# Optimization experiments

Measured on AMD Instinct MI355X. Metric: run time of the kernel, lower is better.

Reference implementation:

```python
import jax, jax.numpy as jnp
import numpy as np

A_CONST = 0.4
C_CONST = 500.0
N_BINS = 10


def entropy(w):
    # Faithful to the torch helper: n=10 half-open bins [min+i*s, min+(i+1)*s);
    # the maximum element falls outside the last bin, as in the original.
    x = w.reshape(-1)
    lo = x.min()
    hi = x.max()
    scale = (hi - lo) / N_BINS
    i = jnp.arange(N_BINS, dtype=x.dtype)
    lower = lo + i * scale            # [n]
    upper = lo + (i + 1.0) * scale    # [n]
    in_bin = (x[None, :] >= lower[:, None]) & (x[None, :] < upper[:, None])  # [n, len]
    p = jnp.sum(in_bin, axis=1).astype(jnp.float32) / x.shape[0]
    return jnp.sum(jnp.where(p > 0, -p * jnp.log(p), 0.0))


def blend_weight(base_w, graft_w, pnet_w):
    # param_direction = |base - graft| passed through bias-free Linear(in, in)
    d = jnp.abs(base_w - graft_w) @ pnet_w.T          # [out, in]
    w_local = jax.nn.sigmoid(d)
    w_global = A_CONST / jnp.pi * jnp.arctan(C_CONST * (entropy(base_w) - entropy(graft_w))) + 0.5
    w_base = w_global * (1.0 - jnp.exp(-w_global * w_local))
    w_graft = (1.0 - w_global) * (1.0 - jnp.exp(-(1.0 - w_global) * (1.0 - w_local)))
    ws = jax.nn.softmax(jnp.stack([w_base, w_graft], axis=-1), axis=-1)  # [out, in, 2]
    return base_w * ws[..., 0] + graft_w * ws[..., 1]


def setup_inputs() -> dict:
    key = jax.random.key(0)
    ks = jax.random.split(key, 9)
    B, D_IN, D_H, D_OUT = 65536, 1024, 512, 1
    return {
        "x": jax.random.normal(ks[0], (B, D_IN), dtype=jnp.float32),
        "w0": jax.random.normal(ks[1], (D_H, D_IN), dtype=jnp.float32) * 0.05,
        "b0": jax.random.normal(ks[2], (D_H,), dtype=jnp.float32) * 0.05,
        "w1": jax.random.normal(ks[3], (D_OUT, D_H), dtype=jnp.float32) * 0.05,
        "b1": jax.random.normal(ks[4], (D_OUT,), dtype=jnp.float32) * 0.05,
        "p0": jax.random.normal(ks[5], (D_IN, D_IN), dtype=jnp.float32) * 0.05,
        "p1": jax.random.normal(ks[6], (D_H, D_H), dtype=jnp.float32) * 0.05,
        "g0": jax.random.normal(ks[7], (D_H, D_IN), dtype=jnp.float32) * 0.05,
        "g1": jax.random.normal(ks[8], (D_OUT, D_H), dtype=jnp.float32) * 0.05,
    }


def reference(x, w0, b0, w1, b1, p0, p1, g0, g1):
    W0 = blend_weight(w0, g0, p0)
    x = jax.nn.relu(x @ W0.T + b0)   # layer 0 + ReLU
    W1 = blend_weight(w1, g1, p1)
    x = x @ W1.T + b1                # layer 1, no activation
    return x
```

## Files before the change

### kernel.cpp

```cpp
#include <hip/hip_runtime.h>
#include <hip/hip_bf16.h>
#include <math.h>


typedef __attribute__((ext_vector_type(8))) short short8;
typedef __attribute__((ext_vector_type(4))) float floatx4;
typedef unsigned short ushort_t;

#define WS_ENT 0
#define WS_MM 4
#define WS_CNT 16
#define WS_W0B_WORD 64
#define WS_W1B_WORD (64 + 262144)

__device__ __forceinline__ unsigned f2ord(float f) {
    unsigned u = __float_as_uint(f);
    return (u & 0x80000000u) ? ~u : (u | 0x80000000u);
}
__device__ __forceinline__ float ord2f(unsigned k) {
    unsigned u = (k & 0x80000000u) ? (k ^ 0x80000000u) : ~k;
    return __uint_as_float(u);
}
__device__ __forceinline__ short f2bf(float f) {
    union { __hip_bfloat16 h; short s; } u;
    u.h = __float2bfloat16(f);
    return u.s;
}
__device__ __forceinline__ float blend_factor(float d, float wg) {
    float wl = 1.0f / (1.0f + expf(-d));
    float wb = wg * (1.0f - expf(-wg * wl));
    float wgr = (1.0f - wg) * (1.0f - expf(-(1.0f - wg) * (1.0f - wl)));
    return 1.0f / (1.0f + expf(-(wb - wgr)));
}
__device__ __forceinline__ float wglobal_from_ent(float eb, float eg) {
    return 0.12732395447351627f * atanf(500.0f * (eb - eg)) + 0.5f;
}
__device__ __forceinline__ void async16(const void* g, void* s) {
    __builtin_amdgcn_global_load_lds(
        (const __attribute__((address_space(1))) unsigned int*)g,
        (__attribute__((address_space(3))) unsigned int*)s, 16, 0, 0);
}

__global__ void init_kernel(unsigned* ws_u, float* out, const float* __restrict__ b1) {
    int gid = blockIdx.x * 256 + threadIdx.x;
    out[gid] = b1[0];
    if (blockIdx.x == 0) {
        int t = threadIdx.x;
        if (t < 4) {
            ws_u[WS_MM + 2 * t] = 0xFFFFFFFFu;
            ws_u[WS_MM + 2 * t + 1] = 0u;
        }
        if (t >= WS_CNT && t < WS_CNT + 40) ws_u[t] = 0u;
    }
}

__device__ __forceinline__ void array_map(int bx, const float* w0, const float* g0,
                                          const float* w1, const float* g1,
                                          int& a, const float*& arr, int& per, int& start) {
    if (bx < 64) { a = 0; arr = w0; per = 524288 / 64; start = bx * per; }
    else if (bx < 128) { a = 1; arr = g0; per = 524288 / 64; start = (bx - 64) * per; }
    else if (bx == 128) { a = 2; arr = w1; per = 512; start = 0; }
    else { a = 3; arr = g1; per = 512; start = 0; }
}

__global__ __launch_bounds__(256) void minmax_kernel(const float* __restrict__ w0,
                                                     const float* __restrict__ g0,
                                                     const float* __restrict__ w1,
                                                     const float* __restrict__ g1,
                                                     unsigned* ws_u) {
    int a, per, start;
    const float* arr;
    array_map(blockIdx.x, w0, g0, w1, g1, a, arr, per, start);
    float mn = INFINITY, mx = -INFINITY;
    for (int i = threadIdx.x; i < per; i += 256) {
        float v = arr[start + i];
        mn = fminf(mn, v);
        mx = fmaxf(mx, v);
    }
#pragma unroll
    for (int off = 32; off > 0; off >>= 1) {
        mn = fminf(mn, __shfl_xor(mn, off));
        mx = fmaxf(mx, __shfl_xor(mx, off));
    }
    __shared__ float smn[4], smx[4];
    int wave = threadIdx.x >> 6, lane = threadIdx.x & 63;
    if (lane == 0) { smn[wave] = mn; smx[wave] = mx; }
    __syncthreads();
    if (threadIdx.x == 0) {
        mn = fminf(fminf(smn[0], smn[1]), fminf(smn[2], smn[3]));
        mx = fmaxf(fmaxf(smx[0], smx[1]), fmaxf(smx[2], smx[3]));
        atomicMin(&ws_u[WS_MM + 2 * a], f2ord(mn));
        atomicMax(&ws_u[WS_MM + 2 * a + 1], f2ord(mx));
    }
}

__global__ __launch_bounds__(256) void hist_kernel(const float* __restrict__ w0,
                                                   const float* __restrict__ g0,
                                                   const float* __restrict__ w1,
                                                   const float* __restrict__ g1,
                                                   unsigned* ws_u) {
    int a, per, start;
    const float* arr;
    array_map(blockIdx.x, w0, g0, w1, g1, a, arr, per, start);
    float lo = ord2f(ws_u[WS_MM + 2 * a]);
    float hi = ord2f(ws_u[WS_MM + 2 * a + 1]);
    float scale = __fdiv_rn(__fsub_rn(hi, lo), 10.0f);
    __shared__ float lower[11];
    __shared__ unsigned cnt[10];
    if (threadIdx.x < 11)
        lower[threadIdx.x] = __fadd_rn(lo, __fmul_rn((float)threadIdx.x, scale));
    if (threadIdx.x < 10) cnt[threadIdx.x] = 0u;
    __syncthreads();
    float inv_scale = 1.0f / scale;
    for (int i = threadIdx.x; i < per; i += 256) {
        float v = arr[start + i];
        int g = (int)floorf((v - lo) * inv_scale);
#pragma unroll
        for (int db = -1; db <= 1; db++) {
            int b = g + db;
            if (b >= 0 && b <= 9 && v >= lower[b] && v < lower[b + 1])
                atomicAdd(&cnt[b], 1u);
        }
    }
    __syncthreads();
    if (threadIdx.x < 10 && cnt[threadIdx.x] > 0)
        atomicAdd(&ws_u[WS_CNT + a * 10 + threadIdx.x], cnt[threadIdx.x]);
}

__global__ void finalize_ent_kernel(unsigned* ws_u) {
    int a = threadIdx.x;
    if (a < 4) {
        float n = (a < 2) ? 524288.0f : 512.0f;
        float ent = 0.0f;
        for (int i = 0; i < 10; i++) {
            float p = __fdiv_rn((float)ws_u[WS_CNT + a * 10 + i], n);
            if (p > 0.0f) ent = __fsub_rn(ent, __fmul_rn(p, logf(p)));
        }
        ((float*)ws_u)[WS_ENT + a] = ent;
    }
}

__global__ __launch_bounds__(256) void blend0_kernel(const float* __restrict__ w0,
                                                     const float* __restrict__ g0,
                                                     const float* __restrict__ p0,
                                                     const float* __restrict__ ws_f,
                                                     ushort_t* __restrict__ W0bb) {
    __shared__ float As[64][17];
    __shared__ float Bs[64][17];
    int tid = threadIdx.x;
    int bo = blockIdx.y * 64;
    int bi = blockIdx.x * 64;
    int tx = tid & 15, ty = tid >> 4;
    int lr = tid >> 2, lc = (tid & 3) * 4;
    float acc[4][4] = {};
    for (int k0 = 0; k0 < 1024; k0 += 16) {
        float4 vw = *(const float4*)&w0[(bo + lr) * 1024 + k0 + lc];
        float4 vg = *(const float4*)&g0[(bo + lr) * 1024 + k0 + lc];
        float4 vp = *(const float4*)&p0[(bi + lr) * 1024 + k0 + lc];
        As[lr][lc + 0] = fabsf(vw.x - vg.x);
        As[lr][lc + 1] = fabsf(vw.y - vg.y);
        As[lr][lc + 2] = fabsf(vw.z - vg.z);
        As[lr][lc + 3] = fabsf(vw.w - vg.w);
        Bs[lr][lc + 0] = vp.x;
        Bs[lr][lc + 1] = vp.y;
        Bs[lr][lc + 2] = vp.z;
        Bs[lr][lc + 3] = vp.w;
        __syncthreads();
#pragma unroll
        for (int k = 0; k < 16; k++) {
            float av[4], bv[4];
#pragma unroll
            for (int r = 0; r < 4; r++) av[r] = As[ty * 4 + r][k];
#pragma unroll
            for (int c = 0; c < 4; c++) bv[c] = Bs[tx * 4 + c][k];
#pragma unroll
            for (int r = 0; r < 4; r++)
#pragma unroll
                for (int c = 0; c < 4; c++) acc[r][c] += av[r] * bv[c];
        }
        __syncthreads();
    }
    float wg = wglobal_from_ent(ws_f[WS_ENT + 0], ws_f[WS_ENT + 1]);
#pragma unroll
    for (int r = 0; r < 4; r++) {
#pragma unroll
        for (int c = 0; c < 4; c++) {
            int o = bo + ty * 4 + r, i = bi + tx * 4 + c;
            float s0 = blend_factor(acc[r][c], wg);
            float v = w0[o * 1024 + i] * s0 + g0[o * 1024 + i] * (1.0f - s0);
            W0bb[o * 1024 + i] = (ushort_t)f2bf(v);
        }
    }
}

__global__ __launch_bounds__(256) void blend1_kernel(const float* __restrict__ w1,
                                                     const float* __restrict__ g1,
                                                     const float* __restrict__ p1,
                                                     const float* __restrict__ ws_f,
                                                     float* __restrict__ W1b) {
    __shared__ float diff[512];
    int tid = threadIdx.x;
    for (int i = tid; i < 512; i += 256) diff[i] = fabsf(w1[i] - g1[i]);
    __syncthreads();
    int wave = tid >> 6, lane = tid & 63;
    int i = blockIdx.x * 4 + wave;
    float acc = 0.0f;
#pragma unroll
    for (int j = 0; j < 8; j++) {
        int k = lane + 64 * j;
        acc += diff[k] * p1[i * 512 + k];
    }
#pragma unroll
    for (int off = 32; off > 0; off >>= 1) acc += __shfl_xor(acc, off);
    if (lane == 0) {
        float wg = wglobal_from_ent(ws_f[WS_ENT + 2], ws_f[WS_ENT + 3]);
        float s0 = blend_factor(acc, wg);
        W1b[i] = w1[i] * s0 + g1[i] * (1.0f - s0);
    }
}

__global__ __launch_bounds__(256) void main_mfma(const float* __restrict__ x,
                                                 const float* __restrict__ b0,
                                                 const ushort_t* __restrict__ W0bb,
                                                 const float* __restrict__ W1b,
                                                 float* __restrict__ out) {
    __shared__ ushort_t As[128 * 40];
    __shared__ ushort_t Bs[128 * 32];
    int tid = threadIdx.x;
    int w = tid >> 6, l = tid & 63;
    int row0 = blockIdx.x * 128, col0 = blockIdx.y * 128;
    int wm = w & 1, wn = w >> 1;
    int m_in = l & 15, kq = l >> 4;

    floatx4 acc[4][4];
    const floatx4 zero = {0.0f, 0.0f, 0.0f, 0.0f};
#pragma unroll
    for (int tm = 0; tm < 4; tm++)
#pragma unroll
        for (int tn = 0; tn < 4; tn++) acc[tm][tn] = zero;

    int arow = tid >> 1;
    int acol = (tid & 1) * 16;
    const float* xbase = x + (size_t)(row0 + arow) * 1024 + acol;
    ushort_t* awr = &As[arow * 40 + acol];
    const ushort_t* bsrc0 = W0bb + (size_t)(col0 + w * 16 + (l >> 2)) * 1024 + (l & 3) * 8;
    const ushort_t* bsrc1 = bsrc0 + (size_t)64 * 1024;
    ushort_t* bdst0 = &Bs[w * 512];
    ushort_t* bdst1 = &Bs[2048 + w * 512];

#pragma unroll 1
    for (int k0 = 0; k0 < 1024; k0 += 32) {
        async16(bsrc0 + k0, bdst0);
        async16(bsrc1 + k0, bdst1);
        float4 v0 = *(const float4*)(xbase + k0);
        float4 v1 = *(const float4*)(xbase + k0 + 4);
        float4 v2 = *(const float4*)(xbase + k0 + 8);
        float4 v3 = *(const float4*)(xbase + k0 + 12);
        short8 s0, s1;
        s0[0] = f2bf(v0.x); s0[1] = f2bf(v0.y); s0[2] = f2bf(v0.z); s0[3] = f2bf(v0.w);
        s0[4] = f2bf(v1.x); s0[5] = f2bf(v1.y); s0[6] = f2bf(v1.z); s0[7] = f2bf(v1.w);
        s1[0] = f2bf(v2.x); s1[1] = f2bf(v2.y); s1[2] = f2bf(v2.z); s1[3] = f2bf(v2.w);
        s1[4] = f2bf(v3.x); s1[5] = f2bf(v3.y); s1[6] = f2bf(v3.z); s1[7] = f2bf(v3.w);
        *(short8*)(awr) = s0;
        *(short8*)(awr + 8) = s1;
        __syncthreads();
        short8 af[4], bfr[4];
#pragma unroll
        for (int tm = 0; tm < 4; tm++)
            af[tm] = *(const short8*)&As[(wm * 64 + tm * 16 + m_in) * 40 + kq * 8];
#pragma unroll
        for (int tn = 0; tn < 4; tn++)
            bfr[tn] = *(const short8*)&Bs[(wn * 64 + tn * 16 + m_in) * 32 + kq * 8];
#pragma unroll
        for (int tm = 0; tm < 4; tm++)
#pragma unroll
            for (int tn = 0; tn < 4; tn++)
                acc[tm][tn] = __builtin_amdgcn_mfma_f32_16x16x32_bf16(
                    af[tm], bfr[tn], acc[tm][tn], 0, 0, 0);
        __syncthreads();
    }

    float b0v[4], w1v[4];
#pragma unroll
    for (int tn = 0; tn < 4; tn++) {
        int h = col0 + wn * 64 + tn * 16 + m_in;
        b0v[tn] = b0[h];
        w1v[tn] = W1b[h];
    }
#pragma unroll
    for (int tm = 0; tm < 4; tm++) {
#pragma unroll
        for (int reg = 0; reg < 4; reg++) {
            float s = 0.0f;
#pragma unroll
            for (int tn = 0; tn < 4; tn++) {
                float y = acc[tm][tn][reg] + b0v[tn];
                y = fmaxf(y, 0.0f);
                s += y * w1v[tn];
            }
            s += __shfl_xor(s, 1);
            s += __shfl_xor(s, 2);
            s += __shfl_xor(s, 4);
            s += __shfl_xor(s, 8);
            if (m_in == 0)
                atomicAdd(&out[row0 + wm * 64 + tm * 16 + kq * 4 + reg], s);
        }
    }
}

extern "C" void kernel_launch(void* const* d_in, const int* in_sizes, int n_in,
                              void* d_out, int out_size, void* d_ws, size_t ws_size,
                              hipStream_t stream) {
    const float* x = (const float*)d_in[0];
    const float* w0 = (const float*)d_in[1];
    const float* b0 = (const float*)d_in[2];
    const float* w1 = (const float*)d_in[3];
    const float* b1 = (const float*)d_in[4];
    const float* p0 = (const float*)d_in[5];
    const float* p1 = (const float*)d_in[6];
    const float* g0 = (const float*)d_in[7];
    const float* g1 = (const float*)d_in[8];
    float* out = (float*)d_out;
    unsigned* ws_u = (unsigned*)d_ws;
    float* ws_f = (float*)d_ws;
    ushort_t* W0bb = (ushort_t*)(ws_u + WS_W0B_WORD);
    float* W1b = ws_f + WS_W1B_WORD;

    init_kernel<<<256, 256, 0, stream>>>(ws_u, out, b1);
    minmax_kernel<<<130, 256, 0, stream>>>(w0, g0, w1, g1, ws_u);
    hist_kernel<<<130, 256, 0, stream>>>(w0, g0, w1, g1, ws_u);
    finalize_ent_kernel<<<1, 64, 0, stream>>>(ws_u);
    blend0_kernel<<<dim3(16, 8), 256, 0, stream>>>(w0, g0, p0, ws_f, W0bb);
    blend1_kernel<<<128, 256, 0, stream>>>(w1, g1, p1, ws_f, W1b);
    main_mfma<<<dim3(512, 4), 256, 0, stream>>>(x, b0, W0bb, W1b, out);
}
```

Before: 627.4 us.

## Fuse prep stages into cooperative kernel and widen main GEMM tile to full hidden dim

Merges the init, min/max, histogram, entropy and both blend kernels into one cooperative kernel separated by grid-wide syncs, cutting five launches. The main MFMA kernel now gives each block 64 rows across all 512 hidden units, with a swizzled LDS layout for W0 and register prefetch of x. The layer-1 dot product is reduced in shared memory and written directly, replacing global atomics and the output init pass. In exchange it adds grid-sync overhead, raises LDS and register use per block (fewer resident blocks), and each block now streams the whole W0 matrix.

```diff
diff --git a/kernel.cpp b/kernel.cpp
--- a/kernel.cpp
+++ b/kernel.cpp
@@ -1,6 +1,9 @@
 #include <hip/hip_runtime.h>
 #include <hip/hip_bf16.h>
+#include <hip/hip_cooperative_groups.h>
 #include <math.h>
+
+namespace cg = cooperative_groups;
 
 
 typedef __attribute__((ext_vector_type(8))) short short8;
@@ -39,19 +42,6 @@
     __builtin_amdgcn_global_load_lds(
         (const __attribute__((address_space(1))) unsigned int*)g,
         (__attribute__((address_space(3))) unsigned int*)s, 16, 0, 0);
-}
-
-__global__ void init_kernel(unsigned* ws_u, float* out, const float* __restrict__ b1) {
-    int gid = blockIdx.x * 256 + threadIdx.x;
-    out[gid] = b1[0];
-    if (blockIdx.x == 0) {
-        int t = threadIdx.x;
-        if (t < 4) {
-            ws_u[WS_MM + 2 * t] = 0xFFFFFFFFu;
-            ws_u[WS_MM + 2 * t + 1] = 0u;
-        }
-        if (t >= WS_CNT && t < WS_CNT + 40) ws_u[t] = 0u;
-    }
 }
 
 __device__ __forceinline__ void array_map(int bx, const float* w0, const float* g0,
@@ -63,227 +53,232 @@
     else { a = 3; arr = g1; per = 512; start = 0; }
 }
 
-__global__ __launch_bounds__(256) void minmax_kernel(const float* __restrict__ w0,
-                                                     const float* __restrict__ g0,
-                                                     const float* __restrict__ w1,
-                                                     const float* __restrict__ g1,
-                                                     unsigned* ws_u) {
-    int a, per, start;
-    const float* arr;
-    array_map(blockIdx.x, w0, g0, w1, g1, a, arr, per, start);
-    float mn = INFINITY, mx = -INFINITY;
-    for (int i = threadIdx.x; i < per; i += 256) {
-        float v = arr[start + i];
-        mn = fminf(mn, v);
-        mx = fmaxf(mx, v);
-    }
-#pragma unroll
-    for (int off = 32; off > 0; off >>= 1) {
-        mn = fminf(mn, __shfl_xor(mn, off));
-        mx = fmaxf(mx, __shfl_xor(mx, off));
-    }
+__global__ __launch_bounds__(256) void prep_kernel(
+    const float* __restrict__ w0, const float* __restrict__ g0,
+    const float* __restrict__ w1, const float* __restrict__ g1,
+    const float* __restrict__ p0, const float* __restrict__ p1,
+    unsigned* ws_u, ushort_t* __restrict__ W0bb, float* __restrict__ W1b) {
+    cg::grid_group grid = cg::this_grid();
+    float* ws_f = (float*)ws_u;
+    int bx = blockIdx.x, tid = threadIdx.x;
+    int wave = tid >> 6, lane = tid & 63;
+
     __shared__ float smn[4], smx[4];
-    int wave = threadIdx.x >> 6, lane = threadIdx.x & 63;
-    if (lane == 0) { smn[wave] = mn; smx[wave] = mx; }
-    __syncthreads();
-    if (threadIdx.x == 0) {
-        mn = fminf(fminf(smn[0], smn[1]), fminf(smn[2], smn[3]));
-        mx = fmaxf(fmaxf(smx[0], smx[1]), fmaxf(smx[2], smx[3]));
-        atomicMin(&ws_u[WS_MM + 2 * a], f2ord(mn));
-        atomicMax(&ws_u[WS_MM + 2 * a + 1], f2ord(mx));
-    }
-}
-
-__global__ __launch_bounds__(256) void hist_kernel(const float* __restrict__ w0,
-                                                   const float* __restrict__ g0,
-                                                   const float* __restrict__ w1,
-                                                   const float* __restrict__ g1,
-                                                   unsigned* ws_u) {
-    int a, per, start;
-    const float* arr;
-    array_map(blockIdx.x, w0, g0, w1, g1, a, arr, per, start);
-    float lo = ord2f(ws_u[WS_MM + 2 * a]);
-    float hi = ord2f(ws_u[WS_MM + 2 * a + 1]);
-    float scale = __fdiv_rn(__fsub_rn(hi, lo), 10.0f);
     __shared__ float lower[11];
     __shared__ unsigned cnt[10];
-    if (threadIdx.x < 11)
-        lower[threadIdx.x] = __fadd_rn(lo, __fmul_rn((float)threadIdx.x, scale));
-    if (threadIdx.x < 10) cnt[threadIdx.x] = 0u;
-    __syncthreads();
-    float inv_scale = 1.0f / scale;
-    for (int i = threadIdx.x; i < per; i += 256) {
-        float v = arr[start + i];
-        int g = (int)floorf((v - lo) * inv_scale);
-#pragma unroll
-        for (int db = -1; db <= 1; db++) {
-            int b = g + db;
-            if (b >= 0 && b <= 9 && v >= lower[b] && v < lower[b + 1])
-                atomicAdd(&cnt[b], 1u);
-        }
-    }
-    __syncthreads();
-    if (threadIdx.x < 10 && cnt[threadIdx.x] > 0)
-        atomicAdd(&ws_u[WS_CNT + a * 10 + threadIdx.x], cnt[threadIdx.x]);
-}
-
-__global__ void finalize_ent_kernel(unsigned* ws_u) {
-    int a = threadIdx.x;
-    if (a < 4) {
+    __shared__ float diff[512];
+    __shared__ float As[64][17];
+    __shared__ float Bs[64][17];
+
+    if (bx == 0) {
+        if (tid < 4) {
+            ws_u[WS_MM + 2 * tid] = 0xFFFFFFFFu;
+            ws_u[WS_MM + 2 * tid + 1] = 0u;
+        }
+        if (tid >= WS_CNT && tid < WS_CNT + 40) ws_u[tid] = 0u;
+    }
+    grid.sync();
+
+    {
+        int a, per, start;
+        const float* arr;
+        array_map(bx, w0, g0, w1, g1, a, arr, per, start);
+        float mn = INFINITY, mx = -INFINITY;
+        for (int i = tid; i < per; i += 256) {
+            float v = arr[start + i];
+            mn = fminf(mn, v);
+            mx = fmaxf(mx, v);
+        }
+#pragma unroll
+        for (int off = 32; off > 0; off >>= 1) {
+            mn = fminf(mn, __shfl_xor(mn, off));
+            mx = fmaxf(mx, __shfl_xor(mx, off));
+        }
+        if (lane == 0) { smn[wave] = mn; smx[wave] = mx; }
+        __syncthreads();
+        if (tid == 0) {
+            mn = fminf(fminf(smn[0], smn[1]), fminf(smn[2], smn[3]));
+            mx = fmaxf(fmaxf(smx[0], smx[1]), fmaxf(smx[2], smx[3]));
+            atomicMin(&ws_u[WS_MM + 2 * a], f2ord(mn));
+            atomicMax(&ws_u[WS_MM + 2 * a + 1], f2ord(mx));
+        }
+    }
+    grid.sync();
+
+    {
+        int a, per, start;
+        const float* arr;
+        array_map(bx, w0, g0, w1, g1, a, arr, per, start);
+        float lo = ord2f(ws_u[WS_MM + 2 * a]);
+        float hi = ord2f(ws_u[WS_MM + 2 * a + 1]);
+        float scale = __fdiv_rn(__fsub_rn(hi, lo), 10.0f);
+        if (tid < 11) lower[tid] = __fadd_rn(lo, __fmul_rn((float)tid, scale));
+        if (tid < 10) cnt[tid] = 0u;
+        __syncthreads();
+        float inv_scale = 1.0f / scale;
+        for (int i = tid; i < per; i += 256) {
+            float v = arr[start + i];
+            int g = (int)floorf((v - lo) * inv_scale);
+#pragma unroll
+            for (int db = -1; db <= 1; db++) {
+                int b = g + db;
+                if (b >= 0 && b <= 9 && v >= lower[b] && v < lower[b + 1])
+                    atomicAdd(&cnt[b], 1u);
+            }
+        }
+        __syncthreads();
+        if (tid < 10 && cnt[tid] > 0)
+            atomicAdd(&ws_u[WS_CNT + a * 10 + tid], cnt[tid]);
+    }
+    grid.sync();
+
+    if (bx == 0 && tid < 4) {
+        int a = tid;
         float n = (a < 2) ? 524288.0f : 512.0f;
         float ent = 0.0f;
         for (int i = 0; i < 10; i++) {
             float p = __fdiv_rn((float)ws_u[WS_CNT + a * 10 + i], n);
             if (p > 0.0f) ent = __fsub_rn(ent, __fmul_rn(p, logf(p)));
         }
-        ((float*)ws_u)[WS_ENT + a] = ent;
-    }
-}
-
-__global__ __launch_bounds__(256) void blend0_kernel(const float* __restrict__ w0,
-                                                     const float* __restrict__ g0,
-                                                     const float* __restrict__ p0,
-                                                     const float* __restrict__ ws_f,
-                                                     ushort_t* __restrict__ W0bb) {
-    __shared__ float As[64][17];
-    __shared__ float Bs[64][17];
-    int tid = threadIdx.x;
-    int bo = blockIdx.y * 64;
-    int bi = blockIdx.x * 64;
-    int tx = tid & 15, ty = tid >> 4;
-    int lr = tid >> 2, lc = (tid & 3) * 4;
-    float acc[4][4] = {};
-    for (int k0 = 0; k0 < 1024; k0 += 16) {
-        float4 vw = *(const float4*)&w0[(bo + lr) * 1024 + k0 + lc];
-        float4 vg = *(const float4*)&g0[(bo + lr) * 1024 + k0 + lc];
-        float4 vp = *(const float4*)&p0[(bi + lr) * 1024 + k0 + lc];
-        As[lr][lc + 0] = fabsf(vw.x - vg.x);
-        As[lr][lc + 1] = fabsf(vw.y - vg.y);
-        As[lr][lc + 2] = fabsf(vw.z - vg.z);
-        As[lr][lc + 3] = fabsf(vw.w - vg.w);
-        Bs[lr][lc + 0] = vp.x;
-        Bs[lr][lc + 1] = vp.y;
-        Bs[lr][lc + 2] = vp.z;
-        Bs[lr][lc + 3] = vp.w;
-        __syncthreads();
-#pragma unroll
-        for (int k = 0; k < 16; k++) {
-            float av[4], bv[4];
-#pragma unroll
-            for (int r = 0; r < 4; r++) av[r] = As[ty * 4 + r][k];
-#pragma unroll
-            for (int c = 0; c < 4; c++) bv[c] = Bs[tx * 4 + c][k];
-#pragma unroll
-            for (int r = 0; r < 4; r++)
-#pragma unroll
-                for (int c = 0; c < 4; c++) acc[r][c] += av[r] * bv[c];
-        }
-        __syncthreads();
-    }
-    float wg = wglobal_from_ent(ws_f[WS_ENT + 0], ws_f[WS_ENT + 1]);
-#pragma unroll
-    for (int r = 0; r < 4; r++) {
-#pragma unroll
-        for (int c = 0; c < 4; c++) {
-            int o = bo + ty * 4 + r, i = bi + tx * 4 + c;
-            float s0 = blend_factor(acc[r][c], wg);
-            float v = w0[o * 1024 + i] * s0 + g0[o * 1024 + i] * (1.0f - s0);
-            W0bb[o * 1024 + i] = (ushort_t)f2bf(v);
-        }
-    }
-}
-
-__global__ __launch_bounds__(256) void blend1_kernel(const float* __restrict__ w1,
-                                                     const float* __restrict__ g1,
-                                                     const float* __restrict__ p1,
-                                                     const float* __restrict__ ws_f,
-                                                     float* __restrict__ W1b) {
-    __shared__ float diff[512];
-    int tid = threadIdx.x;
-    for (int i = tid; i < 512; i += 256) diff[i] = fabsf(w1[i] - g1[i]);
-    __syncthreads();
-    int wave = tid >> 6, lane = tid & 63;
-    int i = blockIdx.x * 4 + wave;
-    float acc = 0.0f;
-#pragma unroll
-    for (int j = 0; j < 8; j++) {
-        int k = lane + 64 * j;
-        acc += diff[k] * p1[i * 512 + k];
-    }
-#pragma unroll
-    for (int off = 32; off > 0; off >>= 1) acc += __shfl_xor(acc, off);
-    if (lane == 0) {
-        float wg = wglobal_from_ent(ws_f[WS_ENT + 2], ws_f[WS_ENT + 3]);
-        float s0 = blend_factor(acc, wg);
-        W1b[i] = w1[i] * s0 + g1[i] * (1.0f - s0);
-    }
-}
-
-__global__ __launch_bounds__(256) void main_mfma(const float* __restrict__ x,
-                                                 const float* __restrict__ b0,
-                                                 const ushort_t* __restrict__ W0bb,
-                                                 const float* __restrict__ W1b,
-                                                 float* __restrict__ out) {
-    __shared__ ushort_t As[128 * 40];
-    __shared__ ushort_t Bs[128 * 32];
+        ws_f[WS_ENT + a] = ent;
+    }
+    grid.sync();
+
+    if (bx < 128) {
+        for (int i = tid; i < 512; i += 256) diff[i] = fabsf(w1[i] - g1[i]);
+        __syncthreads();
+        int i = bx * 4 + wave;
+        float acc = 0.0f;
+#pragma unroll
+        for (int j = 0; j < 8; j++) {
+            int k = lane + 64 * j;
+            acc += diff[k] * p1[i * 512 + k];
+        }
+#pragma unroll
+        for (int off = 32; off > 0; off >>= 1) acc += __shfl_xor(acc, off);
+        if (lane == 0) {
+            float wg = wglobal_from_ent(ws_f[WS_ENT + 2], ws_f[WS_ENT + 3]);
+            float s0 = blend_factor(acc, wg);
+            W1b[i] = w1[i] * s0 + g1[i] * (1.0f - s0);
+        }
+        __syncthreads();
+    }
+
+    if (bx < 128) {
+        int bo = (bx >> 4) * 64;
+        int bi = (bx & 15) * 64;
+        int tx = tid & 15, ty = tid >> 4;
+        int lr = tid >> 2, lc = (tid & 3) * 4;
+        float acc[4][4] = {};
+        for (int k0 = 0; k0 < 1024; k0 += 16) {
+            float4 vw = *(const float4*)&w0[(bo + lr) * 1024 + k0 + lc];
+            float4 vg = *(const float4*)&g0[(bo + lr) * 1024 + k0 + lc];
+            float4 vp = *(const float4*)&p0[(bi + lr) * 1024 + k0 + lc];
+            As[lr][lc + 0] = fabsf(vw.x - vg.x);
+            As[lr][lc + 1] = fabsf(vw.y - vg.y);
+            As[lr][lc + 2] = fabsf(vw.z - vg.z);
+            As[lr][lc + 3] = fabsf(vw.w - vg.w);
+            Bs[lr][lc + 0] = vp.x;
+            Bs[lr][lc + 1] = vp.y;
+            Bs[lr][lc + 2] = vp.z;
+            Bs[lr][lc + 3] = vp.w;
+            __syncthreads();
+#pragma unroll
+            for (int k = 0; k < 16; k++) {
+                float av[4], bv[4];
+#pragma unroll
+                for (int r = 0; r < 4; r++) av[r] = As[ty * 4 + r][k];
+#pragma unroll
+                for (int c = 0; c < 4; c++) bv[c] = Bs[tx * 4 + c][k];
+#pragma unroll
+                for (int r = 0; r < 4; r++)
+#pragma unroll
+                    for (int c = 0; c < 4; c++) acc[r][c] += av[r] * bv[c];
+            }
+            __syncthreads();
+        }
+        float wg = wglobal_from_ent(ws_f[WS_ENT + 0], ws_f[WS_ENT + 1]);
+#pragma unroll
+        for (int r = 0; r < 4; r++) {
+#pragma unroll
+            for (int c = 0; c < 4; c++) {
+                int o = bo + ty * 4 + r, i = bi + tx * 4 + c;
+                float s0 = blend_factor(acc[r][c], wg);
+                float v = w0[o * 1024 + i] * s0 + g0[o * 1024 + i] * (1.0f - s0);
+                W0bb[o * 1024 + i] = (ushort_t)f2bf(v);
+            }
+        }
+    }
+}
+
+__global__ __launch_bounds__(256) void main_mfma(
+    const float* __restrict__ x, const float* __restrict__ b0,
+    const float* __restrict__ b1, const ushort_t* __restrict__ W0bb,
+    const float* __restrict__ W1b, float* __restrict__ out) {
+    __shared__ ushort_t As[64 * 40];
+    __shared__ ushort_t Bs[512 * 32];
+    __shared__ float red[4 * 64];
+
     int tid = threadIdx.x;
     int w = tid >> 6, l = tid & 63;
-    int row0 = blockIdx.x * 128, col0 = blockIdx.y * 128;
-    int wm = w & 1, wn = w >> 1;
     int m_in = l & 15, kq = l >> 4;
-
-    floatx4 acc[4][4];
+    int row0 = blockIdx.x * 64;
+
+    floatx4 acc[4][8];
     const floatx4 zero = {0.0f, 0.0f, 0.0f, 0.0f};
 #pragma unroll
     for (int tm = 0; tm < 4; tm++)
 #pragma unroll
-        for (int tn = 0; tn < 4; tn++) acc[tm][tn] = zero;
-
-    int arow = tid >> 1;
-    int acol = (tid & 1) * 16;
-    const float* xbase = x + (size_t)(row0 + arow) * 1024 + acol;
-    ushort_t* awr = &As[arow * 40 + acol];
-    const ushort_t* bsrc0 = W0bb + (size_t)(col0 + w * 16 + (l >> 2)) * 1024 + (l & 3) * 8;
-    const ushort_t* bsrc1 = bsrc0 + (size_t)64 * 1024;
-    ushort_t* bdst0 = &Bs[w * 512];
-    ushort_t* bdst1 = &Bs[2048 + w * 512];
+        for (int tn = 0; tn < 8; tn++) acc[tm][tn] = zero;
+
+    int ar = tid >> 2, akc = (tid & 3) * 8;
+    const float* xptr = x + (size_t)(row0 + ar) * 1024 + akc;
+    ushort_t* awr = &As[ar * 40 + akc];
+
+    int c_src = ((l & 3) - (l >> 3)) & 3;
+    const ushort_t* bsrc = W0bb + (size_t)(w * 16 + (l >> 2)) * 1024 + c_src * 8;
+    ushort_t* bdst = &Bs[w * 512];
+
+    float4 xa = *(const float4*)(xptr);
+    float4 xb = *(const float4*)(xptr + 4);
 
 #pragma unroll 1
     for (int k0 = 0; k0 < 1024; k0 += 32) {
-        async16(bsrc0 + k0, bdst0);
-        async16(bsrc1 + k0, bdst1);
-        float4 v0 = *(const float4*)(xbase + k0);
-        float4 v1 = *(const float4*)(xbase + k0 + 4);
-        float4 v2 = *(const float4*)(xbase + k0 + 8);
-        float4 v3 = *(const float4*)(xbase + k0 + 12);
-        short8 s0, s1;
-        s0[0] = f2bf(v0.x); s0[1] = f2bf(v0.y); s0[2] = f2bf(v0.z); s0[3] = f2bf(v0.w);
-        s0[4] = f2bf(v1.x); s0[5] = f2bf(v1.y); s0[6] = f2bf(v1.z); s0[7] = f2bf(v1.w);
-        s1[0] = f2bf(v2.x); s1[1] = f2bf(v2.y); s1[2] = f2bf(v2.z); s1[3] = f2bf(v2.w);
-        s1[4] = f2bf(v3.x); s1[5] = f2bf(v3.y); s1[6] = f2bf(v3.z); s1[7] = f2bf(v3.w);
-        *(short8*)(awr) = s0;
-        *(short8*)(awr + 8) = s1;
-        __syncthreads();
-        short8 af[4], bfr[4];
+#pragma unroll
+        for (int i = 0; i < 8; i++)
+            async16(bsrc + i * 65536 + k0, bdst + i * 2048);
+        short8 s8;
+        s8[0] = f2bf(xa.x); s8[1] = f2bf(xa.y); s8[2] = f2bf(xa.z); s8[3] = f2bf(xa.w);
+        s8[4] = f2bf(xb.x); s8[5] = f2bf(xb.y); s8[6] = f2bf(xb.z); s8[7] = f2bf(xb.w);
+        *(short8*)awr = s8;
+        if (k0 + 32 < 1024) {
+            xa = *(const float4*)(xptr + k0 + 32);
+            xb = *(const float4*)(xptr + k0 + 36);
+        }
+        __syncthreads();
+        short8 af[4], bfr[8];
 #pragma unroll
         for (int tm = 0; tm < 4; tm++)
-            af[tm] = *(const short8*)&As[(wm * 64 + tm * 16 + m_in) * 40 + kq * 8];
-#pragma unroll
-        for (int tn = 0; tn < 4; tn++)
-            bfr[tn] = *(const short8*)&Bs[(wn * 64 + tn * 16 + m_in) * 32 + kq * 8];
+            af[tm] = *(const short8*)&As[(tm * 16 + m_in) * 40 + kq * 8];
+        int s = (kq + (m_in >> 1)) & 3;
+#pragma unroll
+        for (int tn = 0; tn < 8; tn++) {
+            int h = w * 128 + tn * 16 + m_in;
+            bfr[tn] = *(const short8*)&Bs[h * 32 + s * 8];
+        }
 #pragma unroll
         for (int tm = 0; tm < 4; tm++)
 #pragma unroll
-            for (int tn = 0; tn < 4; tn++)
+            for (int tn = 0; tn < 8; tn++)
                 acc[tm][tn] = __builtin_amdgcn_mfma_f32_16x16x32_bf16(
                     af[tm], bfr[tn], acc[tm][tn], 0, 0, 0);
         __syncthreads();
     }
 
-    float b0v[4], w1v[4];
-#pragma unroll
-    for (int tn = 0; tn < 4; tn++) {
-        int h = col0 + wn * 64 + tn * 16 + m_in;
+    float b0v[8], w1v[8];
+#pragma unroll
+    for (int tn = 0; tn < 8; tn++) {
+        int h = w * 128 + tn * 16 + m_in;
         b0v[tn] = b0[h];
         w1v[tn] = W1b[h];
     }
@@ -293,7 +288,7 @@
         for (int reg = 0; reg < 4; reg++) {
             float s = 0.0f;
 #pragma unroll
-            for (int tn = 0; tn < 4; tn++) {
+            for (int tn = 0; tn < 8; tn++) {
                 float y = acc[tm][tn][reg] + b0v[tn];
                 y = fmaxf(y, 0.0f);
                 s += y * w1v[tn];
@@ -302,10 +297,13 @@
             s += __shfl_xor(s, 2);
             s += __shfl_xor(s, 4);
             s += __shfl_xor(s, 8);
-            if (m_in == 0)
-                atomicAdd(&out[row0 + wm * 64 + tm * 16 + kq * 4 + reg], s);
-        }
-    }
+            if (m_in == 0) red[w * 64 + tm * 16 + kq * 4 + reg] = s;
+        }
+    }
+    __syncthreads();
+    if (tid < 64)
+        out[row0 + tid] =
+            red[tid] + red[64 + tid] + red[128 + tid] + red[192 + tid] + b1[0];
 }
 
 extern "C" void kernel_launch(void* const* d_in, const int* in_sizes, int n_in,
@@ -326,11 +324,8 @@
     ushort_t* W0bb = (ushort_t*)(ws_u + WS_W0B_WORD);
     float* W1b = ws_f + WS_W1B_WORD;
 
-    init_kernel<<<256, 256, 0, stream>>>(ws_u, out, b1);
-    minmax_kernel<<<130, 256, 0, stream>>>(w0, g0, w1, g1, ws_u);
-    hist_kernel<<<130, 256, 0, stream>>>(w0, g0, w1, g1, ws_u);
-    finalize_ent_kernel<<<1, 64, 0, stream>>>(ws_u);
-    blend0_kernel<<<dim3(16, 8), 256, 0, stream>>>(w0, g0, p0, ws_f, W0bb);
-    blend1_kernel<<<128, 256, 0, stream>>>(w1, g1, p1, ws_f, W1b);
-    main_mfma<<<dim3(512, 4), 256, 0, stream>>>(x, b0, W0bb, W1b, out);
-}
+    void* args[] = {(void*)&w0, (void*)&g0, (void*)&w1, (void*)&g1,
+                    (void*)&p0, (void*)&p1, (void*)&ws_u, (void*)&W0bb, (void*)&W1b};
+    hipLaunchCooperativeKernel((void*)prep_kernel, dim3(130), dim3(256), args, 0, stream);
+    main_mfma<<<1024, 256, 0, stream>>>(x, b0, b1, W0bb, W1b, out);
+}
```

Measured after the change: 693.5 us. +10.5%, slower.
